# Kernel tuning notes

Measured on AMD Instinct MI355X. Metric: run time of the kernel, lower is better.

## Reference

```python
import jax, jax.numpy as jnp
import numpy as np

DIM_MODEL = 512
DIM_HEAD = 64


def setup_inputs() -> dict:
    key = jax.random.key(0)
    ks = jax.random.split(key, 7)
    B, S = 4, 4096
    x = jax.random.normal(ks[0], (B, S, DIM_MODEL), dtype=jnp.float32)
    mask = jnp.ones((B, 1, S), dtype=jnp.int32)
    # torch Linear init: U(-1/sqrt(fan_in), 1/sqrt(fan_in)); stored as (in, out) for x @ W
    bound = 1.0 / np.sqrt(DIM_MODEL)
    Wq = jax.random.uniform(ks[1], (DIM_MODEL, DIM_HEAD), minval=-bound, maxval=bound, dtype=jnp.float32)
    bq = jax.random.uniform(ks[2], (DIM_HEAD,), minval=-bound, maxval=bound, dtype=jnp.float32)
    Wk = jax.random.uniform(ks[3], (DIM_MODEL, DIM_HEAD), minval=-bound, maxval=bound, dtype=jnp.float32)
    bk = jax.random.uniform(ks[4], (DIM_HEAD,), minval=-bound, maxval=bound, dtype=jnp.float32)
    Wv = jax.random.uniform(ks[5], (DIM_MODEL, DIM_HEAD), minval=-bound, maxval=bound, dtype=jnp.float32)
    bv = jax.random.uniform(ks[6], (DIM_HEAD,), minval=-bound, maxval=bound, dtype=jnp.float32)
    return {"x": x, "mask": mask, "Wq": Wq, "bq": bq, "Wk": Wk, "bk": bk, "Wv": Wv, "bv": bv}


def reference(x, mask, Wq, bq, Wk, bk, Wv, bv):
    # single-head QKV projection
    q = x @ Wq + bq  # (B, S, Dh)
    k = x @ Wk + bk
    v = x @ Wv + bv
    dot_scale = jnp.sqrt(jnp.float32(DIM_HEAD))
    # explicit O(S^2) score matrix, softmax over keys
    scores = jnp.einsum("bqd,bkd->bqk", q, k) / dot_scale  # (B, S, S)
    attn = jax.nn.softmax(scores, axis=-1)
    # faithful to source: mask applied AFTER softmax with -inf fill
    attn = jnp.where(mask == 0, jnp.float32(-jnp.inf), attn)
    return jnp.einsum("bqk,bkd->bqd", attn, v)  # (B, S, Dh)
```

## Files before the change

### kernel.cpp

```cpp
#include <hip/hip_runtime.h>
#include <hip/hip_bf16.h>

typedef _Float16 half8v __attribute__((ext_vector_type(8)));
typedef _Float16 half4v __attribute__((ext_vector_type(4)));
typedef _Float16 half2v __attribute__((ext_vector_type(2)));
typedef __fp16   fp16x2 __attribute__((ext_vector_type(2)));
typedef __attribute__((ext_vector_type(4))) float floatx4;

#define LOG2E_OVER_8 0.18033688011112042f


__global__ __launch_bounds__(256) void wtrans_k(const float* __restrict__ Wq,
                                                const float* __restrict__ Wk,
                                                const float* __restrict__ Wv,
                                                _Float16* __restrict__ Wt) {
    int idx = blockIdx.x * 256 + threadIdx.x;
    int p = idx >> 15, rem = idx & 32767;
    int k = rem >> 6;
    int n = rem & 63;
    const float* W = (p == 0) ? Wq : ((p == 1) ? Wk : Wv);
    int ctg = p * 4 + (n >> 4), m = n & 15;
    int kc = k >> 5, quad = (k >> 3) & 3, j = k & 7;
    Wt[(((ctg << 4) + kc) * 64 + (quad << 4) + m) * 8 + j] = (_Float16)W[k * 64 + n];
}

#define XS_STRIDE 536
__global__ __launch_bounds__(256) void proj_k(const float* __restrict__ x,
                                              const _Float16* __restrict__ Wt,
                                              const float* __restrict__ bq,
                                              const float* __restrict__ bk,
                                              const float* __restrict__ bv,
                                              _Float16* __restrict__ Qh,
                                              _Float16* __restrict__ Kh,
                                              _Float16* __restrict__ Vh) {
    __shared__ _Float16 xs[2][16 * XS_STRIDE];

    int tid = threadIdx.x, l = tid & 63, wv = tid >> 6;
    int m = l & 15, quad = l >> 4;
    int row0 = blockIdx.x * 32;

#pragma unroll
    for (int s = 0; s < 2; s++)
#pragma unroll
        for (int i = 0; i < 8; i++) {
            int idx = tid + i * 256;
            int row = idx >> 7, c4 = idx & 127;
            float4 v = *(const float4*)(x + (row0 + s * 16 + row) * 512 + c4 * 4);
            union { half2v h[2]; uint2 u; } cv;
            cv.h[0][0] = (_Float16)v.x; cv.h[0][1] = (_Float16)v.y;
            cv.h[1][0] = (_Float16)v.z; cv.h[1][1] = (_Float16)v.w;
            *(uint2*)(xs[s] + row * XS_STRIDE + c4 * 4) = cv.u;
        }
    __syncthreads();

    const _Float16* arow0 = xs[0] + m * XS_STRIDE + quad * 8;
    const _Float16* arow1 = xs[1] + m * XS_STRIDE + quad * 8;

    floatx4 acc[2][3];
#pragma unroll
    for (int s = 0; s < 2; s++)
#pragma unroll
        for (int i = 0; i < 3; i++) acc[s][i] = (floatx4)(0.f);

#pragma unroll 4
    for (int kc = 0; kc < 16; kc++) {
        half8v a0 = *(const half8v*)(arow0 + kc * 32);
        half8v a1 = *(const half8v*)(arow1 + kc * 32);
#pragma unroll
        for (int ct = 0; ct < 3; ct++) {
            int ctg = wv * 3 + ct;
            half8v b = *(const half8v*)(Wt + (((ctg << 4) + kc) * 64 + l) * 8);
            acc[0][ct] = __builtin_amdgcn_mfma_f32_16x16x32_f16(a0, b, acc[0][ct], 0, 0, 0);
            acc[1][ct] = __builtin_amdgcn_mfma_f32_16x16x32_f16(a1, b, acc[1][ct], 0, 0, 0);
        }
    }

#pragma unroll
    for (int s = 0; s < 2; s++) {
        int rowb = row0 + s * 16;
#pragma unroll
        for (int ct = 0; ct < 3; ct++) {
            int ctg = wv * 3 + ct;
            int col = ctg * 16 + m;
            float bias = (ctg < 4) ? bq[col] : ((ctg < 8) ? bk[col - 64] : bv[col - 128]);
            if (ctg < 8) {
                _Float16* dst = (ctg < 4) ? Qh : Kh;
                float scl = (ctg < 4) ? LOG2E_OVER_8 : 1.0f;
                int dd = (ctg & 3) * 16 + m;
                int c = dd >> 5, quadQ = (dd >> 3) & 3, j = dd & 7;
#pragma unroll
                for (int r = 0; r < 4; r++) {
                    int row = rowb + quad * 4 + r;
                    int chunk = ((row >> 4) << 1) + c;
                    dst[(chunk * 64 + quadQ * 16 + (row & 15)) * 8 + j] =
                        (_Float16)((acc[s][ct][r] + bias) * scl);
                }
            } else {
                int dt = ctg - 8;
                int t64 = rowb >> 6, ktp = (rowb >> 5) & 1, half = (rowb >> 4) & 1;
                int chunk = t64 * 8 + dt * 2 + ktp;
                union { _Float16 h[4]; unsigned long long u; } pk;
#pragma unroll
                for (int r = 0; r < 4; r++) pk.h[r] = (_Float16)(acc[s][ct][r] + bias);
                *(unsigned long long*)(Vh + (chunk * 64 + quad * 16 + m) * 8 + half * 4) = pk.u;
            }
        }
    }
}

template <int NT>
__global__ __launch_bounds__(256) void attn_k(const _Float16* __restrict__ Qh,
                                              const _Float16* __restrict__ Kh,
                                              const _Float16* __restrict__ Vh,
                                              const int* __restrict__ mask,
                                              _Float16* __restrict__ Np,
                                              float* __restrict__ Dp,
                                              int gshift) {
    __shared__ float T[4][16 * 68];

    int tid = threadIdx.x, l = tid & 63, wv = tid >> 6;
    int m = l & 15, quad = l >> 4;
    int bid = blockIdx.x;
    int grp = bid & ((1 << gshift) - 1), qblk = bid >> gshift;
    int os = grp >> 2, b = grp & 3;
    int q0 = qblk * 128 + wv * 32;

    const int* maskb = mask + b * 4096 + os * (NT * 64);
    int az = 0;
#pragma unroll
    for (int i = 0; i < NT; i++) az |= (maskb[l + i * 64] == 0);
    const bool hasz = __any(az);

    int qt_g = (b * 4096 + q0) >> 4;
    half8v qf[2][2];
#pragma unroll
    for (int qt = 0; qt < 2; qt++)
#pragma unroll
        for (int c = 0; c < 2; c++)
            qf[qt][c] = *(const half8v*)(Qh + (((qt_g + qt) * 2 + c) * 64 + l) * 8);

    int tb0 = (b * 64 + os * NT) * 512;
    const uint4* kh4 = (const uint4*)Kh + tb0;
    const uint4* vh4 = (const uint4*)Vh + tb0;

    floatx4 oacc[2][4];
#pragma unroll
    for (int qt = 0; qt < 2; qt++)
#pragma unroll
        for (int dt = 0; dt < 4; dt++) oacc[qt][dt] = (floatx4)(0.f);
    float dl[2] = {0.f, 0.f};

#pragma unroll 2
    for (int t = 0; t < NT; t++) {
        const uint4* kt4 = kh4 + t * 512;
        const uint4* vt4 = vh4 + t * 512;
        uint4 vv[4];
#pragma unroll
        for (int sub = 0; sub < 4; sub++) {
            union { uint4 u; half8v h; } ku0, ku1;
            ku0.u = kt4[(sub * 2 + 0) * 64 + l];
            ku1.u = kt4[(sub * 2 + 1) * 64 + l];
            if ((sub & 1) == 0) {
#pragma unroll
                for (int dt = 0; dt < 4; dt++)
                    vv[dt] = vt4[(dt * 2 + (sub >> 1)) * 64 + l];
            }
            half4v pb[2];
#pragma unroll
            for (int qt = 0; qt < 2; qt++) {
                floatx4 sf = (floatx4)(0.f);
                sf = __builtin_amdgcn_mfma_f32_16x16x32_f16(ku0.h, qf[qt][0], sf, 0, 0, 0);
                sf = __builtin_amdgcn_mfma_f32_16x16x32_f16(ku1.h, qf[qt][1], sf, 0, 0, 0);
                float p0 = exp2f(sf[0]), p1 = exp2f(sf[1]);
                float p2 = exp2f(sf[2]), p3 = exp2f(sf[3]);
                dl[qt] += (p0 + p1) + (p2 + p3);
                if (hasz) {
                    int kg = t * 64 + sub * 16 + quad * 4;
                    if (maskb[kg + 0] == 0) p0 = -__builtin_inff();
                    if (maskb[kg + 1] == 0) p1 = -__builtin_inff();
                    if (maskb[kg + 2] == 0) p2 = -__builtin_inff();
                    if (maskb[kg + 3] == 0) p3 = -__builtin_inff();
                }
                union { fp16x2 h[2]; half4v h4; } pu;
                pu.h[0] = __builtin_amdgcn_cvt_pkrtz(p0, p1);
                pu.h[1] = __builtin_amdgcn_cvt_pkrtz(p2, p3);
                pb[qt] = pu.h4;
            }
#pragma unroll
            for (int dt = 0; dt < 4; dt++) {
                union { uint4 u; half4v h[2]; } vc; vc.u = vv[dt];
                half4v va = vc.h[sub & 1];
                oacc[0][dt] = __builtin_amdgcn_mfma_f32_16x16x16f16(va, pb[0], oacc[0][dt], 0, 0, 0);
                oacc[1][dt] = __builtin_amdgcn_mfma_f32_16x16x16f16(va, pb[1], oacc[1][dt], 0, 0, 0);
            }
        }
    }

    float* Tw = &T[wv][0];
    int rowb = os * 16384 + b * 4096 + q0;
#pragma unroll
    for (int qt = 0; qt < 2; qt++) {
        float dqt = dl[qt];
        dqt += __shfl_xor(dqt, 16, 64);
        dqt += __shfl_xor(dqt, 32, 64);
        if (l < 16) Dp[rowb + qt * 16 + l] = dqt;
#pragma unroll
        for (int dt = 0; dt < 4; dt++)
#pragma unroll
            for (int r = 0; r < 4; r++)
                Tw[m * 68 + dt * 16 + quad * 4 + r] = oacc[qt][dt][r];
        __builtin_amdgcn_s_waitcnt(0);
#pragma unroll
        for (int g = 0; g < 4; g++) {
            int idx = g * 64 + l;
            int row = idx >> 4, c4 = (idx & 15) * 4;
            float4 v = *(const float4*)(Tw + row * 68 + c4);
            union { half4v h; unsigned long long u; } pk;
            pk.h[0] = (_Float16)v.x; pk.h[1] = (_Float16)v.y;
            pk.h[2] = (_Float16)v.z; pk.h[3] = (_Float16)v.w;
            *(unsigned long long*)(Np + (size_t)(rowb + qt * 16 + row) * 64 + c4) = pk.u;
        }
        __builtin_amdgcn_s_waitcnt(0);
    }
}

__global__ __launch_bounds__(256) void combine_k(const _Float16* __restrict__ Np,
                                                 const float* __restrict__ Dp,
                                                 float* __restrict__ out,
                                                 int spl) {
    int g4 = blockIdx.x * 256 + threadIdx.x;
    int row = g4 >> 4;
    float4 nu = make_float4(0.f, 0.f, 0.f, 0.f);
    float d = 0.f;
    for (int sp = 0; sp < spl; sp++) {
        union { unsigned long long u; half4v h; } v;
        v.u = *(const unsigned long long*)(Np + ((size_t)sp << 20) + (size_t)g4 * 4);
        nu.x += (float)v.h[0]; nu.y += (float)v.h[1];
        nu.z += (float)v.h[2]; nu.w += (float)v.h[3];
        d += Dp[sp * 16384 + row];
    }
    float inv = 1.0f / d;
    ((float4*)out)[g4] = make_float4(nu.x * inv, nu.y * inv, nu.z * inv, nu.w * inv);
}

extern "C" void kernel_launch(void* const* d_in, const int* in_sizes, int n_in,
                              void* d_out, int out_size, void* d_ws, size_t ws_size,
                              hipStream_t stream) {
    const float* x  = (const float*)d_in[0];
    const int* mask = (const int*)d_in[1];
    const float* Wq = (const float*)d_in[2];
    const float* bq = (const float*)d_in[3];
    const float* Wk = (const float*)d_in[4];
    const float* bk = (const float*)d_in[5];
    const float* Wv = (const float*)d_in[6];
    const float* bv = (const float*)d_in[7];
    float* out = (float*)d_out;

    char* ws = (char*)d_ws;
    _Float16* Wt = (_Float16*)(ws);
    _Float16* Qh = (_Float16*)(ws + 0x40000);
    _Float16* Kh = (_Float16*)(ws + 0x240000);
    _Float16* Vh = (_Float16*)(ws + 0x440000);
    float*    Dp = (float*)(ws + 0x640000);
    _Float16* Np = (_Float16*)(ws + 0x740000);

    wtrans_k<<<384, 256, 0, stream>>>(Wq, Wk, Wv, Wt);
    proj_k<<<512, 256, 0, stream>>>(x, Wt, bq, bk, bv, Qh, Kh, Vh);
    attn_k<8><<<32 * 32, 256, 0, stream>>>(Qh, Kh, Vh, mask, Np, Dp, 5);
    combine_k<<<1024, 256, 0, stream>>>(Np, Dp, out, 8);
}
```

Before: 137.9 us.

## Double-buffer K/V tiles in LDS via async global-to-LDS loads

Each key/value tile is now loaded once per block straight into shared memory with global_load_lds, instead of every wave fetching it separately from global memory. Two buffers are used so the next tile's load overlaps with the MFMA work on the current tile. The score staging area now reuses the same LDS allocation. This cuts redundant L2 traffic across the four waves, at the cost of a block-wide barrier on every tile and a reliance on the barrier also waiting for the async loads to finish.

```diff
diff --git a/kernel.cpp b/kernel.cpp
--- a/kernel.cpp
+++ b/kernel.cpp
@@ -9,6 +9,13 @@
 
 #define LOG2E_OVER_8 0.18033688011112042f
 
+
+__device__ __forceinline__ void gload_lds16(const void* g, void* l) {
+    __builtin_amdgcn_global_load_lds(
+        (const __attribute__((address_space(1))) void*)(unsigned long long)g,
+        (__attribute__((address_space(3))) void*)(unsigned)(unsigned long long)l,
+        16, 0, 0);
+}
 
 __global__ __launch_bounds__(256) void wtrans_k(const float* __restrict__ Wq,
                                                 const float* __restrict__ Wk,
@@ -116,7 +123,7 @@
                                               _Float16* __restrict__ Np,
                                               float* __restrict__ Dp,
                                               int gshift) {
-    __shared__ float T[4][16 * 68];
+    __shared__ __align__(16) uint4 stage_lds[2][1024];
 
     int tid = threadIdx.x, l = tid & 63, wv = tid >> 6;
     int m = l & 15, quad = l >> 4;
@@ -150,10 +157,31 @@
         for (int dt = 0; dt < 4; dt++) oacc[qt][dt] = (floatx4)(0.f);
     float dl[2] = {0.f, 0.f};
 
+#pragma unroll
+    for (int i = 0; i < 2; i++) {
+        int idx = wv * 128 + i * 64 + l;
+        gload_lds16(kh4 + idx, &stage_lds[0][0] + idx);
+        gload_lds16(vh4 + idx, &stage_lds[0][512] + idx);
+    }
+    __syncthreads();
+
 #pragma unroll 2
     for (int t = 0; t < NT; t++) {
-        const uint4* kt4 = kh4 + t * 512;
-        const uint4* vt4 = vh4 + t * 512;
+        int cur = t & 1;
+        if (t + 1 < NT) {
+            const uint4* ksrc = kh4 + (t + 1) * 512;
+            const uint4* vsrc = vh4 + (t + 1) * 512;
+            uint4* kb = &stage_lds[cur ^ 1][0];
+            uint4* vb = &stage_lds[cur ^ 1][512];
+#pragma unroll
+            for (int i = 0; i < 2; i++) {
+                int idx = wv * 128 + i * 64 + l;
+                gload_lds16(ksrc + idx, kb + idx);
+                gload_lds16(vsrc + idx, vb + idx);
+            }
+        }
+        const uint4* kt4 = &stage_lds[cur][0];
+        const uint4* vt4 = &stage_lds[cur][512];
         uint4 vv[4];
 #pragma unroll
         for (int sub = 0; sub < 4; sub++) {
@@ -194,9 +222,10 @@
                 oacc[1][dt] = __builtin_amdgcn_mfma_f32_16x16x16f16(va, pb[1], oacc[1][dt], 0, 0, 0);
             }
         }
-    }
-
-    float* Tw = &T[wv][0];
+        __syncthreads();
+    }
+
+    float* Tw = (float*)&stage_lds[0][0] + wv * (16 * 68);
     int rowb = os * 16384 + b * 4096 + q0;
 #pragma unroll
     for (int qt = 0; qt < 2; qt++) {
```

New measurement: 137.2 us. No clear change (-0.6%).
